# Performance work log

Measured on AMD Instinct MI355X. Metric: run time of the kernel, lower is better.

## Reference

```python
import jax, jax.numpy as jnp
import numpy as np

N_NODES = 50000
N_EDGES = 1_600_000
HID = 64
BN_EPS = 1e-5


def setup_inputs() -> dict:
    key = jax.random.key(0)
    ks = jax.random.split(key, 16)
    x = jax.random.normal(ks[0], (N_NODES, 1), dtype=jnp.float32)
    edge_index = jax.random.randint(ks[1], (2, N_EDGES), 0, N_NODES, dtype=jnp.int32)
    s = 1.0 / np.sqrt(HID)
    # layer 1: 1 -> 64 -> 64
    w1a = jax.random.normal(ks[2], (1, HID), dtype=jnp.float32)
    b1a = jnp.zeros((HID,), jnp.float32)
    w2a = jax.random.normal(ks[3], (HID, HID), dtype=jnp.float32) * s
    b2a = jnp.zeros((HID,), jnp.float32)
    # layers 2-4 stacked: 64 -> 64 -> 64
    w1s = jax.random.normal(ks[4], (3, HID, HID), dtype=jnp.float32) * s
    b1s = jnp.zeros((3, HID), jnp.float32)
    w2s = jax.random.normal(ks[5], (3, HID, HID), dtype=jnp.float32) * s
    b2s = jnp.zeros((3, HID), jnp.float32)
    eps = jnp.zeros((4,), jnp.float32)  # train_eps=True, init 0
    gammas = jnp.ones((4, HID), jnp.float32)
    betas = jnp.zeros((4, HID), jnp.float32)
    fc_w = jax.random.normal(ks[6], (HID, 1), dtype=jnp.float32) * s
    fc_b = jnp.zeros((1,), jnp.float32)
    return {"x": x, "edge_index": edge_index, "w1a": w1a, "b1a": b1a,
            "w2a": w2a, "b2a": b2a, "w1s": w1s, "b1s": b1s, "w2s": w2s,
            "b2s": b2s, "eps": eps, "gammas": gammas, "betas": betas,
            "fc_w": fc_w, "fc_b": fc_b}


def _gin(h, src, dst, e, w1, b1, w2, b2):
    # sum_{j in N(i)} h_j  (messages from src, aggregated at dst)
    agg = jax.ops.segment_sum(h[src], dst, num_segments=N_NODES)
    z = (1.0 + e) * h + agg
    return jax.nn.relu(z @ w1 + b1) @ w2 + b2


def _bn(h, g, b):
    # BatchNorm1d, training mode: biased batch statistics over nodes
    mu = jnp.mean(h, axis=0)
    var = jnp.mean((h - mu) ** 2, axis=0)
    return (h - mu) * jax.lax.rsqrt(var + BN_EPS) * g + b


def reference(x, edge_index, w1a, b1a, w2a, b2a, w1s, b1s, w2s, b2s,
              eps, gammas, betas, fc_w, fc_b):
    src, dst = edge_index[0], edge_index[1]
    h = _bn(jax.nn.relu(_gin(x, src, dst, eps[0], w1a, b1a, w2a, b2a)),
            gammas[0], betas[0])
    for i in range(3):
        h = _bn(jax.nn.relu(_gin(h, src, dst, eps[i + 1],
                                 w1s[i], b1s[i], w2s[i], b2s[i])),
                gammas[i + 1], betas[i + 1])
    return h @ fc_w + fc_b
```

## Files before the change

### kernel.cpp

```cpp
#include <hip/hip_runtime.h>
#include <hip/hip_fp16.h>

#define HID 64
#define BN_EPS 1e-5f
#define WINSH 8
#define WINSZ 256
#define B1 256
#define PIT 72

typedef short bf16x8 __attribute__((ext_vector_type(8)));
typedef float f32x4 __attribute__((ext_vector_type(4)));

__device__ __forceinline__ unsigned short f2b(float f) {
    unsigned int u = __float_as_uint(f);
    u = (u + 0x7FFF + ((u >> 16) & 1)) >> 16;
    return (unsigned short)u;
}
__device__ __forceinline__ float b2f(unsigned short h) {
    return __uint_as_float(((unsigned int)h) << 16);
}
__device__ __forceinline__ f32x4 mfma_bf16(bf16x8 a, bf16x8 b, f32x4 c) {
    return __builtin_amdgcn_mfma_f32_16x16x32_bf16(a, b, c, 0, 0, 0);
}

__global__ __launch_bounds__(256) void prep_kernel(const float* __restrict__ w2a,
                                                   const float* __restrict__ w1s,
                                                   const float* __restrict__ w2s,
                                                   unsigned short* __restrict__ whi,
                                                   unsigned short* __restrict__ wlo,
                                                   float* __restrict__ stats,
                                                   const int* __restrict__ dst,
                                                   int* __restrict__ cnt,
                                                   int E, int nw, int chunk) {
    int blk = blockIdx.x, tid = threadIdx.x;
    if (blk < 7) {
        const float* srcm = (blk == 0) ? w2a : (blk <= 3 ? w1s + (size_t)(blk - 1) * 4096
                                                         : w2s + (size_t)(blk - 4) * 4096);
        unsigned short* dh = whi + (size_t)blk * 4096;
        unsigned short* dl = wlo + (size_t)blk * 4096;
        for (int idx = tid; idx < 4096; idx += 256) {
            int j = idx & 7;
            int lane = (idx >> 3) & 63;
            int ntkh = idx >> 9;
            int nt = ntkh >> 1, kh = ntkh & 1;
            int nc = nt * 16 + (lane & 15);
            int k = kh * 32 + (lane >> 4) * 8 + j;
            float v = srcm[k * 64 + nc];
            unsigned short h = f2b(v);
            dh[idx] = h;
            dl[idx] = f2b(v - b2f(h));
        }
    } else if (blk == 7) {
        stats[tid] = 0.f;
        stats[tid + 256] = 0.f;
    } else {
        __shared__ int c[256];
        int b = blk - 8;
        c[tid] = 0;
        __syncthreads();
        int lo = b * chunk;
        int hi = lo + chunk; if (hi > E) hi = E;
        for (int e = lo + tid; e < hi; e += 256) atomicAdd(&c[dst[e] >> WINSH], 1);
        __syncthreads();
        if (tid < nw) cnt[tid * B1 + b] = c[tid];
    }
}

__global__ __launch_bounds__(256) void scan_a_kernel(const int* __restrict__ in,
                                                     int* __restrict__ partial,
                                                     int* __restrict__ blocksum, int n) {
    __shared__ int sums[256];
    int tid = threadIdx.x;
    int i = blockIdx.x * 256 + tid;
    int v = (i < n) ? in[i] : 0;
    sums[tid] = v;
    __syncthreads();
    for (int off = 1; off < 256; off <<= 1) {
        int t = (tid >= off) ? sums[tid - off] : 0;
        __syncthreads();
        sums[tid] += t;
        __syncthreads();
    }
    if (i < n) partial[i] = sums[tid] - v;
    if (tid == 255) blocksum[blockIdx.x] = sums[255];
}

__global__ __launch_bounds__(256) void scan_b_kernel(const int* __restrict__ blocksum,
                                                     int* __restrict__ blockoff, int nb) {
    __shared__ int s[256];
    __shared__ int carry;
    int tid = threadIdx.x;
    if (tid == 0) carry = 0;
    __syncthreads();
    for (int base = 0; base < nb; base += 256) {
        int i = base + tid;
        int v = (i < nb) ? blocksum[i] : 0;
        s[tid] = v;
        __syncthreads();
        for (int off = 1; off < 256; off <<= 1) {
            int t = (tid >= off) ? s[tid - off] : 0;
            __syncthreads();
            s[tid] += t;
            __syncthreads();
        }
        if (i < nb) blockoff[i] = carry + s[tid] - v;
        __syncthreads();
        if (tid == 0) carry += s[255];
        __syncthreads();
    }
}

__global__ __launch_bounds__(256) void p3_bucket_kernel(const int* __restrict__ src,
                                                        const int* __restrict__ dst,
                                                        const int* __restrict__ cpart,
                                                        const int* __restrict__ blockoff,
                                                        int* __restrict__ ebuf,
                                                        int E, int nw, int chunk) {
    __shared__ int cur[256];
    int tid = threadIdx.x, b = blockIdx.x;
    if (tid < nw) cur[tid] = cpart[tid * B1 + b] + blockoff[tid];
    __syncthreads();
    int lo = b * chunk;
    int hi = lo + chunk; if (hi > E) hi = E;
    for (int e = lo + tid; e < hi; e += 256) {
        int d = dst[e];
        int w = d >> WINSH;
        int pos = atomicAdd(&cur[w], 1);
        ebuf[pos] = src[e] | ((d & (WINSZ - 1)) << 24);
    }
}

__global__ __launch_bounds__(256) void p4_fine_kernel(const int* __restrict__ ebuf,
                                                      const int* __restrict__ cpart,
                                                      const int* __restrict__ blockoff,
                                                      int* __restrict__ csr_src,
                                                      int* __restrict__ rowptr,
                                                      int* __restrict__ deg,
                                                      int E, int n, int nw) {
    __shared__ int fcnt[256];
    __shared__ int foff[256];
    int tid = threadIdx.x, w = blockIdx.x;
    int lo = cpart[w * B1] + blockoff[w];
    int hi = (w + 1 < nw) ? cpart[(w + 1) * B1] + blockoff[w + 1] : E;
    fcnt[tid] = 0;
    __syncthreads();
    for (int e = lo + tid; e < hi; e += 256) atomicAdd(&fcnt[(unsigned)ebuf[e] >> 24], 1);
    __syncthreads();
    int v = fcnt[tid];
    foff[tid] = v;
    __syncthreads();
    for (int off = 1; off < 256; off <<= 1) {
        int t = (tid >= off) ? foff[tid - off] : 0;
        __syncthreads();
        foff[tid] += t;
        __syncthreads();
    }
    int myoff = lo + foff[tid] - v;
    int node = w * WINSZ + tid;
    if (node < n) { rowptr[node] = myoff; deg[node] = v; }
    __syncthreads();
    fcnt[tid] = myoff;
    __syncthreads();
    for (int e = lo + tid; e < hi; e += 256) {
        int p = ebuf[e];
        int pos = atomicAdd(&fcnt[(unsigned)p >> 24], 1);
        csr_src[pos] = p & 0xFFFFFF;
    }
}

__global__ __launch_bounds__(256) void gather1_kernel(const float* __restrict__ x,
                                                      const int* __restrict__ rowptr,
                                                      const int* __restrict__ deg,
                                                      const int* __restrict__ csr_src,
                                                      const float* __restrict__ eps,
                                                      float* __restrict__ zscalar, int n) {
    int node = blockIdx.x * 4 + (threadIdx.x >> 6);
    int lane = threadIdx.x & 63;
    if (node >= n) return;
    int start = __builtin_amdgcn_readfirstlane(rowptr[node]);
    int cnt   = __builtin_amdgcn_readfirstlane(deg[node]);
    float a = 0.f;
    for (int i = lane; i < cnt; i += 64) a += x[csr_src[start + i]];
    for (int off = 32; off > 0; off >>= 1) a += __shfl_xor(a, off);
    if (lane == 0) zscalar[node] = (1.0f + eps[0]) * x[node] + a;
}

__global__ __launch_bounds__(256) void mlp_kernel(const float* __restrict__ zscalar,
                                                  const float* __restrict__ w1a,
                                                  const float* __restrict__ b1a,
                                                  const float* __restrict__ hpre_in,
                                                  const __half* __restrict__ hh_in,
                                                  const float* __restrict__ stats_prev,
                                                  const float* __restrict__ gamma_prev,
                                                  const float* __restrict__ beta_prev,
                                                  const int* __restrict__ rowptr,
                                                  const int* __restrict__ deg,
                                                  const int* __restrict__ csr_src,
                                                  const float* __restrict__ eps,
                                                  int layer,
                                                  const unsigned short* __restrict__ w1h,
                                                  const unsigned short* __restrict__ w1l,
                                                  const float* __restrict__ b1v,
                                                  const unsigned short* __restrict__ w2h,
                                                  const unsigned short* __restrict__ w2l,
                                                  const float* __restrict__ b2v,
                                                  float* __restrict__ hpre_out,
                                                  __half* __restrict__ hh_out,
                                                  float* __restrict__ stats,
                                                  int n, int mode, int write_hh) {
    __shared__ __align__(16) unsigned short Ah[64 * PIT];
    __shared__ __align__(16) unsigned short Al[64 * PIT];
    __shared__ float ssum[64], ssq[64];
    __shared__ float bsc[64], bsh[64];

    int tid = threadIdx.x;
    int base = blockIdx.x * 64;
    int lane = tid & 63;
    int wv = tid >> 6;

    if (tid < 64) { ssum[tid] = 0.f; ssq[tid] = 0.f; }

    if (mode) {
        if (tid < 64) {
            float inv_n = 1.0f / (float)n;
            float mu = stats_prev[tid] * inv_n;
            float var = stats_prev[64 + tid] * inv_n - mu * mu;
            float inv = rsqrtf(var + BN_EPS);
            float sc = gamma_prev[tid] * inv;
            bsc[tid] = sc;
            bsh[tid] = beta_prev[tid] - mu * sc;
        }
        __syncthreads();
        float ep = 1.0f + eps[layer];
        float sc = bsc[lane], sh = bsh[lane];
        for (int r = 0; r < 16; ++r) {
            int node = base + wv * 16 + r;
            float z = 0.f;
            if (node < n) {
                int start = __builtin_amdgcn_readfirstlane(rowptr[node]);
                int cnt   = __builtin_amdgcn_readfirstlane(deg[node]);
                float a0 = 0.f, a1 = 0.f, a2 = 0.f, a3 = 0.f;
                float a4 = 0.f, a5 = 0.f, a6 = 0.f, a7 = 0.f;
                int e = 0;
                for (; e + 8 <= cnt; e += 8) {
                    int s0 = csr_src[start + e + 0];
                    int s1 = csr_src[start + e + 1];
                    int s2 = csr_src[start + e + 2];
                    int s3 = csr_src[start + e + 3];
                    int s4 = csr_src[start + e + 4];
                    int s5 = csr_src[start + e + 5];
                    int s6 = csr_src[start + e + 6];
                    int s7 = csr_src[start + e + 7];
                    a0 += __half2float(hh_in[(size_t)s0 * HID + lane]);
                    a1 += __half2float(hh_in[(size_t)s1 * HID + lane]);
                    a2 += __half2float(hh_in[(size_t)s2 * HID + lane]);
                    a3 += __half2float(hh_in[(size_t)s3 * HID + lane]);
                    a4 += __half2float(hh_in[(size_t)s4 * HID + lane]);
                    a5 += __half2float(hh_in[(size_t)s5 * HID + lane]);
                    a6 += __half2float(hh_in[(size_t)s6 * HID + lane]);
                    a7 += __half2float(hh_in[(size_t)s7 * HID + lane]);
                }
                for (; e < cnt; ++e)
                    a0 += __half2float(hh_in[(size_t)csr_src[start + e] * HID + lane]);
                float sum = ((a0 + a1) + (a2 + a3)) + ((a4 + a5) + (a6 + a7));
                float self = hpre_in[(size_t)node * HID + lane];
                z = fmaf(sc, fmaf(ep, self, sum), sh * (ep + (float)cnt));
            }
            unsigned short h = f2b(z);
            int row = wv * 16 + r;
            Ah[row * PIT + lane] = h;
            Al[row * PIT + lane] = f2b(z - b2f(h));
        }
    } else {
        for (int i = tid; i < 4096; i += 256) {
            int nn = i >> 6, k = i & 63;
            float zv = zscalar[base + nn];
            float v = fmaxf(fmaf(zv, w1a[k], b1a[k]), 0.f);
            unsigned short h = f2b(v);
            Ah[nn * PIT + k] = h;
            Al[nn * PIT + k] = f2b(v - b2f(h));
        }
    }
    __syncthreads();

    int m = lane & 15;
    int q = lane >> 4;
    int m0 = wv * 16;

    const bf16x8* a0h = (const bf16x8*)&Ah[(m0 + m) * PIT + q * 8];
    const bf16x8* a1h = (const bf16x8*)&Ah[(m0 + m) * PIT + 32 + q * 8];
    const bf16x8* a0l = (const bf16x8*)&Al[(m0 + m) * PIT + q * 8];
    const bf16x8* a1l = (const bf16x8*)&Al[(m0 + m) * PIT + 32 + q * 8];

    if (mode) {
        bf16x8 xa0h = *a0h, xa1h = *a1h, xa0l = *a0l, xa1l = *a1l;
        f32x4 acc[4];
#pragma unroll
        for (int nt = 0; nt < 4; ++nt) {
            size_t fo0 = ((size_t)(nt * 2 + 0) * 64 + lane) * 8;
            size_t fo1 = ((size_t)(nt * 2 + 1) * 64 + lane) * 8;
            bf16x8 b0h = *(const bf16x8*)(w1h + fo0);
            bf16x8 b1h_ = *(const bf16x8*)(w1h + fo1);
            bf16x8 b0l = *(const bf16x8*)(w1l + fo0);
            bf16x8 b1l_ = *(const bf16x8*)(w1l + fo1);
            f32x4 c = {0.f, 0.f, 0.f, 0.f};
            c = mfma_bf16(xa0h, b0h, c);
            c = mfma_bf16(xa0h, b0l, c);
            c = mfma_bf16(xa0l, b0h, c);
            c = mfma_bf16(xa1h, b1h_, c);
            c = mfma_bf16(xa1h, b1l_, c);
            c = mfma_bf16(xa1l, b1h_, c);
            acc[nt] = c;
        }
#pragma unroll
        for (int nt = 0; nt < 4; ++nt) {
            int col = nt * 16 + m;
            float bv = b1v[col];
#pragma unroll
            for (int r = 0; r < 4; ++r) {
                int row = m0 + q * 4 + r;
                float T = fmaxf(acc[nt][r] + bv, 0.f);
                unsigned short h = f2b(T);
                Ah[row * PIT + col] = h;
                Al[row * PIT + col] = f2b(T - b2f(h));
            }
        }
    }
    __syncthreads();

    {
        bf16x8 xa0h = *a0h, xa1h = *a1h, xa0l = *a0l, xa1l = *a1l;
        f32x4 acc[4];
#pragma unroll
        for (int nt = 0; nt < 4; ++nt) {
            size_t fo0 = ((size_t)(nt * 2 + 0) * 64 + lane) * 8;
            size_t fo1 = ((size_t)(nt * 2 + 1) * 64 + lane) * 8;
            bf16x8 b0h = *(const bf16x8*)(w2h + fo0);
            bf16x8 b1h_ = *(const bf16x8*)(w2h + fo1);
            bf16x8 b0l = *(const bf16x8*)(w2l + fo0);
            bf16x8 b1l_ = *(const bf16x8*)(w2l + fo1);
            f32x4 c = {0.f, 0.f, 0.f, 0.f};
            c = mfma_bf16(xa0h, b0h, c);
            c = mfma_bf16(xa0h, b0l, c);
            c = mfma_bf16(xa0l, b0h, c);
            c = mfma_bf16(xa1h, b1h_, c);
            c = mfma_bf16(xa1h, b1l_, c);
            c = mfma_bf16(xa1l, b1h_, c);
            acc[nt] = c;
        }
#pragma unroll
        for (int nt = 0; nt < 4; ++nt) {
            int col = nt * 16 + m;
            float bv = b2v[col];
            float cs = 0.f, cq = 0.f;
#pragma unroll
            for (int r = 0; r < 4; ++r) {
                int node = base + m0 + q * 4 + r;
                float h = fmaxf(acc[nt][r] + bv, 0.f);
                if (node < n) {
                    hpre_out[(size_t)node * HID + col] = h;
                    if (write_hh) hh_out[(size_t)node * HID + col] = __float2half(h);
                    cs += h;
                    cq = fmaf(h, h, cq);
                }
            }
            cs += __shfl_xor(cs, 16); cs += __shfl_xor(cs, 32);
            cq += __shfl_xor(cq, 16); cq += __shfl_xor(cq, 32);
            if (q == 0) {
                atomicAdd(&ssum[col], cs);
                atomicAdd(&ssq[col], cq);
            }
        }
    }
    __syncthreads();
    if (tid < 64) {
        atomicAdd(&stats[tid], ssum[tid]);
        atomicAdd(&stats[64 + tid], ssq[tid]);
    }
}

__global__ __launch_bounds__(256) void final_kernel(const float* __restrict__ hpre,
                                                    const float* __restrict__ stats,
                                                    const float* __restrict__ gamma,
                                                    const float* __restrict__ beta,
                                                    const float* __restrict__ fcw,
                                                    const float* __restrict__ fcb,
                                                    float* __restrict__ out, int n) {
    int wave = threadIdx.x >> 6;
    int lane = threadIdx.x & 63;
    int node = blockIdx.x * 4 + wave;
    if (node < n) {
        float inv_n = 1.0f / (float)n;
        float mu = stats[lane] * inv_n;
        float var = stats[64 + lane] * inv_n - mu * mu;
        float inv = rsqrtf(var + BN_EPS);
        float sc = gamma[lane] * inv;
        float sh = beta[lane] - mu * sc;
        float v = hpre[(size_t)node * HID + lane];
        float t = fmaf(v, sc, sh) * fcw[lane];
        for (int off = 32; off > 0; off >>= 1) t += __shfl_xor(t, off);
        if (lane == 0) out[node] = t + fcb[0];
    }
}

extern "C" void kernel_launch(void* const* d_in, const int* in_sizes, int n_in,
                              void* d_out, int out_size, void* d_ws, size_t ws_size,
                              hipStream_t stream) {
    const float* x      = (const float*)d_in[0];
    const int*   ei     = (const int*)d_in[1];
    const float* w1a    = (const float*)d_in[2];
    const float* b1a    = (const float*)d_in[3];
    const float* w2a    = (const float*)d_in[4];
    const float* b2a    = (const float*)d_in[5];
    const float* w1s    = (const float*)d_in[6];
    const float* b1s    = (const float*)d_in[7];
    const float* w2s    = (const float*)d_in[8];
    const float* b2s    = (const float*)d_in[9];
    const float* eps    = (const float*)d_in[10];
    const float* gammas = (const float*)d_in[11];
    const float* betas  = (const float*)d_in[12];
    const float* fcw    = (const float*)d_in[13];
    const float* fcb    = (const float*)d_in[14];
    float* out = (float*)d_out;

    int n = in_sizes[0];
    int E = in_sizes[1] / 2;
    int npad = ((n + 63) / 64) * 64;
    int nblk = npad / 64;

    int nw = (n + WINSZ - 1) >> WINSH;
    int NWB = nw * B1;
    int chunk = (E + B1 - 1) / B1;
    int nbs2 = (NWB + 255) / 256;

    const int* src = ei;
    const int* dst = ei + E;

    char* p = (char*)d_ws;
    float* hpreA   = (float*)p; p += (size_t)npad * HID * 4;
    float* hpreB   = (float*)p; p += (size_t)npad * HID * 4;
    __half* hhA    = (__half*)p; p += (size_t)npad * HID * 2;
    __half* hhB    = (__half*)p; p += (size_t)npad * HID * 2;
    float* zscalar = (float*)p; p += (size_t)npad * 4;
    float* stats   = (float*)p; p += 4 * 128 * 4;
    unsigned short* whi = (unsigned short*)p; p += 7 * 4096 * 2;
    unsigned short* wlo = (unsigned short*)p; p += 7 * 4096 * 2;
    int* deg     = (int*)p; p += (size_t)n * 4;
    int* rowptr  = (int*)p; p += (size_t)n * 4;
    int* csr_src = (int*)p; p += (size_t)E * 4;

    int* ebuf     = (int*)hpreB;
    int* cnt      = ebuf + E;
    int* cpart    = cnt + NWB;
    int* bsum     = cpart + NWB;
    int* blockoff = bsum + nbs2;

    prep_kernel<<<8 + B1, 256, 0, stream>>>(w2a, w1s, w2s, whi, wlo, stats,
                                            dst, cnt, E, nw, chunk);
    scan_a_kernel<<<nbs2, 256, 0, stream>>>(cnt, cpart, bsum, NWB);
    scan_b_kernel<<<1, 256, 0, stream>>>(bsum, blockoff, nbs2);
    p3_bucket_kernel<<<B1, 256, 0, stream>>>(src, dst, cpart, blockoff, ebuf, E, nw, chunk);
    p4_fine_kernel<<<nw, 256, 0, stream>>>(ebuf, cpart, blockoff, csr_src, rowptr, deg,
                                           E, n, nw);

    gather1_kernel<<<(n + 3) / 4, 256, 0, stream>>>(x, rowptr, deg, csr_src, eps, zscalar, n);
    mlp_kernel<<<nblk, 256, 0, stream>>>(zscalar, w1a, b1a,
                                         nullptr, nullptr, nullptr, nullptr, nullptr,
                                         rowptr, deg, csr_src, eps, 0,
                                         whi, wlo, b1a ,
                                         whi , wlo, b2a,
                                         hpreA, hhA, stats, n, 0, 1);

    for (int l = 1; l <= 3; ++l) {
        const float* hin  = (l & 1) ? hpreA : hpreB;
        const __half* hhi = (l & 1) ? hhA : hhB;
        float* hout  = (l & 1) ? hpreB : hpreA;
        __half* hho  = (l & 1) ? hhB : hhA;
        mlp_kernel<<<nblk, 256, 0, stream>>>(nullptr, nullptr, nullptr,
                                             hin, hhi,
                                             stats + (l - 1) * 128,
                                             gammas + (l - 1) * HID,
                                             betas + (l - 1) * HID,
                                             rowptr, deg, csr_src, eps, l,
                                             whi + (size_t)l * 4096,
                                             wlo + (size_t)l * 4096,
                                             b1s + (size_t)(l - 1) * HID,
                                             whi + (size_t)(3 + l) * 4096,
                                             wlo + (size_t)(3 + l) * 4096,
                                             b2s + (size_t)(l - 1) * HID,
                                             hout, hho, stats + l * 128,
                                             n, 1, (l < 3) ? 1 : 0);
    }
    final_kernel<<<(n + 3) / 4, 256, 0, stream>>>(hpreB, stats + 3 * 128,
                                                  gammas + 3 * HID, betas + 3 * HID,
                                                  fcw, fcb, out, n);
}
```

Baseline: 445.0 us.

## Split neighbor gather out of MLP kernel into separate per-node gather kernel

Moves the neighbor aggregation and BN-apply out of the fused MLP kernel into a dedicated gather kernel that gives each node its own wave across many small blocks. The MLP kernel then reads the aggregated z from a global buffer. The goal is more parallelism and better latency hiding for the irregular gather than 16 serial nodes per wave inside a 64-row MFMA block. The cost is an extra full-size float buffer written and read per layer plus extra kernel launches. The h buffers are no longer ping-ponged, which is safe only because the gather finishes before the MLP overwrites h.

```diff
diff --git a/kernel.cpp b/kernel.cpp
--- a/kernel.cpp
+++ b/kernel.cpp
@@ -185,91 +185,85 @@
     if (lane == 0) zscalar[node] = (1.0f + eps[0]) * x[node] + a;
 }
 
-__global__ __launch_bounds__(256) void mlp_kernel(const float* __restrict__ zscalar,
+__global__ __launch_bounds__(256) void gatherz_kernel(const float* __restrict__ hpre,
+                                                      const __half* __restrict__ hh16,
+                                                      const float* __restrict__ stats_prev,
+                                                      const float* __restrict__ gamma_prev,
+                                                      const float* __restrict__ beta_prev,
+                                                      const int* __restrict__ rowptr,
+                                                      const int* __restrict__ deg,
+                                                      const int* __restrict__ csr_src,
+                                                      const float* __restrict__ eps,
+                                                      int layer,
+                                                      float* __restrict__ zbuf, int n) {
+    int lane = threadIdx.x & 63;
+    int node = blockIdx.x * 4 + (threadIdx.x >> 6);
+    float inv_n = 1.0f / (float)n;
+    float mu = stats_prev[lane] * inv_n;
+    float var = stats_prev[64 + lane] * inv_n - mu * mu;
+    float inv = rsqrtf(var + BN_EPS);
+    float sc = gamma_prev[lane] * inv;
+    float sh = beta_prev[lane] - mu * sc;
+    if (node >= n) return;
+    int start = __builtin_amdgcn_readfirstlane(rowptr[node]);
+    int cnt   = __builtin_amdgcn_readfirstlane(deg[node]);
+    float a0 = 0.f, a1 = 0.f, a2 = 0.f, a3 = 0.f;
+    float a4 = 0.f, a5 = 0.f, a6 = 0.f, a7 = 0.f;
+    int e = 0;
+    for (; e + 8 <= cnt; e += 8) {
+        int s0 = csr_src[start + e + 0];
+        int s1 = csr_src[start + e + 1];
+        int s2 = csr_src[start + e + 2];
+        int s3 = csr_src[start + e + 3];
+        int s4 = csr_src[start + e + 4];
+        int s5 = csr_src[start + e + 5];
+        int s6 = csr_src[start + e + 6];
+        int s7 = csr_src[start + e + 7];
+        a0 += __half2float(hh16[(size_t)s0 * HID + lane]);
+        a1 += __half2float(hh16[(size_t)s1 * HID + lane]);
+        a2 += __half2float(hh16[(size_t)s2 * HID + lane]);
+        a3 += __half2float(hh16[(size_t)s3 * HID + lane]);
+        a4 += __half2float(hh16[(size_t)s4 * HID + lane]);
+        a5 += __half2float(hh16[(size_t)s5 * HID + lane]);
+        a6 += __half2float(hh16[(size_t)s6 * HID + lane]);
+        a7 += __half2float(hh16[(size_t)s7 * HID + lane]);
+    }
+    for (; e < cnt; ++e) a0 += __half2float(hh16[(size_t)csr_src[start + e] * HID + lane]);
+    float sum = ((a0 + a1) + (a2 + a3)) + ((a4 + a5) + (a6 + a7));
+    float ep = 1.0f + eps[layer];
+    float self = hpre[(size_t)node * HID + lane];
+    zbuf[(size_t)node * HID + lane] =
+        fmaf(sc, fmaf(ep, self, sum), sh * (ep + (float)cnt));
+}
+
+__global__ __launch_bounds__(256) void mlp_kernel(const float* __restrict__ zin,
+                                                  const float* __restrict__ zscalar,
                                                   const float* __restrict__ w1a,
                                                   const float* __restrict__ b1a,
-                                                  const float* __restrict__ hpre_in,
-                                                  const __half* __restrict__ hh_in,
-                                                  const float* __restrict__ stats_prev,
-                                                  const float* __restrict__ gamma_prev,
-                                                  const float* __restrict__ beta_prev,
-                                                  const int* __restrict__ rowptr,
-                                                  const int* __restrict__ deg,
-                                                  const int* __restrict__ csr_src,
-                                                  const float* __restrict__ eps,
-                                                  int layer,
                                                   const unsigned short* __restrict__ w1h,
                                                   const unsigned short* __restrict__ w1l,
                                                   const float* __restrict__ b1v,
                                                   const unsigned short* __restrict__ w2h,
                                                   const unsigned short* __restrict__ w2l,
                                                   const float* __restrict__ b2v,
-                                                  float* __restrict__ hpre_out,
-                                                  __half* __restrict__ hh_out,
+                                                  float* __restrict__ hpre,
+                                                  __half* __restrict__ hh16,
                                                   float* __restrict__ stats,
                                                   int n, int mode, int write_hh) {
     __shared__ __align__(16) unsigned short Ah[64 * PIT];
     __shared__ __align__(16) unsigned short Al[64 * PIT];
     __shared__ float ssum[64], ssq[64];
-    __shared__ float bsc[64], bsh[64];
 
     int tid = threadIdx.x;
     int base = blockIdx.x * 64;
-    int lane = tid & 63;
-    int wv = tid >> 6;
-
-    if (tid < 64) { ssum[tid] = 0.f; ssq[tid] = 0.f; }
 
     if (mode) {
-        if (tid < 64) {
-            float inv_n = 1.0f / (float)n;
-            float mu = stats_prev[tid] * inv_n;
-            float var = stats_prev[64 + tid] * inv_n - mu * mu;
-            float inv = rsqrtf(var + BN_EPS);
-            float sc = gamma_prev[tid] * inv;
-            bsc[tid] = sc;
-            bsh[tid] = beta_prev[tid] - mu * sc;
-        }
-        __syncthreads();
-        float ep = 1.0f + eps[layer];
-        float sc = bsc[lane], sh = bsh[lane];
-        for (int r = 0; r < 16; ++r) {
-            int node = base + wv * 16 + r;
-            float z = 0.f;
-            if (node < n) {
-                int start = __builtin_amdgcn_readfirstlane(rowptr[node]);
-                int cnt   = __builtin_amdgcn_readfirstlane(deg[node]);
-                float a0 = 0.f, a1 = 0.f, a2 = 0.f, a3 = 0.f;
-                float a4 = 0.f, a5 = 0.f, a6 = 0.f, a7 = 0.f;
-                int e = 0;
-                for (; e + 8 <= cnt; e += 8) {
-                    int s0 = csr_src[start + e + 0];
-                    int s1 = csr_src[start + e + 1];
-                    int s2 = csr_src[start + e + 2];
-                    int s3 = csr_src[start + e + 3];
-                    int s4 = csr_src[start + e + 4];
-                    int s5 = csr_src[start + e + 5];
-                    int s6 = csr_src[start + e + 6];
-                    int s7 = csr_src[start + e + 7];
-                    a0 += __half2float(hh_in[(size_t)s0 * HID + lane]);
-                    a1 += __half2float(hh_in[(size_t)s1 * HID + lane]);
-                    a2 += __half2float(hh_in[(size_t)s2 * HID + lane]);
-                    a3 += __half2float(hh_in[(size_t)s3 * HID + lane]);
-                    a4 += __half2float(hh_in[(size_t)s4 * HID + lane]);
-                    a5 += __half2float(hh_in[(size_t)s5 * HID + lane]);
-                    a6 += __half2float(hh_in[(size_t)s6 * HID + lane]);
-                    a7 += __half2float(hh_in[(size_t)s7 * HID + lane]);
-                }
-                for (; e < cnt; ++e)
-                    a0 += __half2float(hh_in[(size_t)csr_src[start + e] * HID + lane]);
-                float sum = ((a0 + a1) + (a2 + a3)) + ((a4 + a5) + (a6 + a7));
-                float self = hpre_in[(size_t)node * HID + lane];
-                z = fmaf(sc, fmaf(ep, self, sum), sh * (ep + (float)cnt));
-            }
-            unsigned short h = f2b(z);
-            int row = wv * 16 + r;
-            Ah[row * PIT + lane] = h;
-            Al[row * PIT + lane] = f2b(z - b2f(h));
+        for (int i = tid; i < 4096; i += 256) {
+            int nn = i >> 6, k = i & 63;
+            float v = zin[(size_t)(base + nn) * HID + k];
+            unsigned short h = f2b(v);
+            Ah[nn * PIT + k] = h;
+            Al[nn * PIT + k] = f2b(v - b2f(h));
         }
     } else {
         for (int i = tid; i < 4096; i += 256) {
@@ -281,11 +275,13 @@
             Al[nn * PIT + k] = f2b(v - b2f(h));
         }
     }
-    __syncthreads();
-
-    int m = lane & 15;
-    int q = lane >> 4;
-    int m0 = wv * 16;
+    if (tid < 64) { ssum[tid] = 0.f; ssq[tid] = 0.f; }
+    __syncthreads();
+
+    int l = tid & 63;
+    int m = l & 15;
+    int q = l >> 4;
+    int m0 = (tid >> 6) * 16;
 
     const bf16x8* a0h = (const bf16x8*)&Ah[(m0 + m) * PIT + q * 8];
     const bf16x8* a1h = (const bf16x8*)&Ah[(m0 + m) * PIT + 32 + q * 8];
@@ -297,8 +293,8 @@
         f32x4 acc[4];
 #pragma unroll
         for (int nt = 0; nt < 4; ++nt) {
-            size_t fo0 = ((size_t)(nt * 2 + 0) * 64 + lane) * 8;
-            size_t fo1 = ((size_t)(nt * 2 + 1) * 64 + lane) * 8;
+            size_t fo0 = ((size_t)(nt * 2 + 0) * 64 + l) * 8;
+            size_t fo1 = ((size_t)(nt * 2 + 1) * 64 + l) * 8;
             bf16x8 b0h = *(const bf16x8*)(w1h + fo0);
             bf16x8 b1h_ = *(const bf16x8*)(w1h + fo1);
             bf16x8 b0l = *(const bf16x8*)(w1l + fo0);
@@ -333,8 +329,8 @@
         f32x4 acc[4];
 #pragma unroll
         for (int nt = 0; nt < 4; ++nt) {
-            size_t fo0 = ((size_t)(nt * 2 + 0) * 64 + lane) * 8;
-            size_t fo1 = ((size_t)(nt * 2 + 1) * 64 + lane) * 8;
+            size_t fo0 = ((size_t)(nt * 2 + 0) * 64 + l) * 8;
+            size_t fo1 = ((size_t)(nt * 2 + 1) * 64 + l) * 8;
             bf16x8 b0h = *(const bf16x8*)(w2h + fo0);
             bf16x8 b1h_ = *(const bf16x8*)(w2h + fo1);
             bf16x8 b0l = *(const bf16x8*)(w2l + fo0);
@@ -358,8 +354,8 @@
                 int node = base + m0 + q * 4 + r;
                 float h = fmaxf(acc[nt][r] + bv, 0.f);
                 if (node < n) {
-                    hpre_out[(size_t)node * HID + col] = h;
-                    if (write_hh) hh_out[(size_t)node * HID + col] = __float2half(h);
+                    hpre[(size_t)node * HID + col] = h;
+                    if (write_hh) hh16[(size_t)node * HID + col] = __float2half(h);
                     cs += h;
                     cq = fmaf(h, h, cq);
                 }
@@ -437,10 +433,9 @@
     const int* dst = ei + E;
 
     char* p = (char*)d_ws;
-    float* hpreA   = (float*)p; p += (size_t)npad * HID * 4;
-    float* hpreB   = (float*)p; p += (size_t)npad * HID * 4;
-    __half* hhA    = (__half*)p; p += (size_t)npad * HID * 2;
-    __half* hhB    = (__half*)p; p += (size_t)npad * HID * 2;
+    float* zbuf    = (float*)p; p += (size_t)npad * HID * 4;
+    float* hpre    = (float*)p; p += (size_t)npad * HID * 4;
+    __half* hh16   = (__half*)p; p += (size_t)npad * HID * 2;
     float* zscalar = (float*)p; p += (size_t)npad * 4;
     float* stats   = (float*)p; p += 4 * 128 * 4;
     unsigned short* whi = (unsigned short*)p; p += 7 * 4096 * 2;
@@ -449,7 +444,7 @@
     int* rowptr  = (int*)p; p += (size_t)n * 4;
     int* csr_src = (int*)p; p += (size_t)E * 4;
 
-    int* ebuf     = (int*)hpreB;
+    int* ebuf     = (int*)zbuf;
     int* cnt      = ebuf + E;
     int* cpart    = cnt + NWB;
     int* bsum     = cpart + NWB;
@@ -464,34 +459,28 @@
                                            E, n, nw);
 
     gather1_kernel<<<(n + 3) / 4, 256, 0, stream>>>(x, rowptr, deg, csr_src, eps, zscalar, n);
-    mlp_kernel<<<nblk, 256, 0, stream>>>(zscalar, w1a, b1a,
-                                         nullptr, nullptr, nullptr, nullptr, nullptr,
-                                         rowptr, deg, csr_src, eps, 0,
+    mlp_kernel<<<nblk, 256, 0, stream>>>(zbuf, zscalar, w1a, b1a,
                                          whi, wlo, b1a ,
                                          whi , wlo, b2a,
-                                         hpreA, hhA, stats, n, 0, 1);
+                                         hpre, hh16, stats, n, 0, 1);
 
     for (int l = 1; l <= 3; ++l) {
-        const float* hin  = (l & 1) ? hpreA : hpreB;
-        const __half* hhi = (l & 1) ? hhA : hhB;
-        float* hout  = (l & 1) ? hpreB : hpreA;
-        __half* hho  = (l & 1) ? hhB : hhA;
-        mlp_kernel<<<nblk, 256, 0, stream>>>(nullptr, nullptr, nullptr,
-                                             hin, hhi,
-                                             stats + (l - 1) * 128,
-                                             gammas + (l - 1) * HID,
-                                             betas + (l - 1) * HID,
-                                             rowptr, deg, csr_src, eps, l,
+        gatherz_kernel<<<(n + 3) / 4, 256, 0, stream>>>(hpre, hh16,
+                                                        stats + (l - 1) * 128,
+                                                        gammas + (l - 1) * HID,
+                                                        betas + (l - 1) * HID,
+                                                        rowptr, deg, csr_src, eps, l, zbuf, n);
+        mlp_kernel<<<nblk, 256, 0, stream>>>(zbuf, zscalar, w1a, b1a,
                                              whi + (size_t)l * 4096,
                                              wlo + (size_t)l * 4096,
                                              b1s + (size_t)(l - 1) * HID,
                                              whi + (size_t)(3 + l) * 4096,
                                              wlo + (size_t)(3 + l) * 4096,
                                              b2s + (size_t)(l - 1) * HID,
-                                             hout, hho, stats + l * 128,
+                                             hpre, hh16, stats + l * 128,
                                              n, 1, (l < 3) ? 1 : 0);
     }
-    final_kernel<<<(n + 3) / 4, 256, 0, stream>>>(hpreB, stats + 3 * 128,
+    final_kernel<<<(n + 3) / 4, 256, 0, stream>>>(hpre, stats + 3 * 128,
                                                   gammas + 3 * HID, betas + 3 * HID,
                                                   fcw, fcb, out, n);
 }
```

Measured after the change: 388.8 us. 1.14x faster.
